# Kernel optimization log

Measured on AMD Instinct MI355X. Metric: run time of the kernel, lower is better.

## Reference

```python
import jax, jax.numpy as jnp
import numpy as np

N_NODES = 100000
N_EDGES = 1600000
D = 128
D_FF = 2 * D
BN_EPS = 1e-5


def setup_inputs() -> dict:
    key = jax.random.key(0)
    ks = jax.random.split(key, 16)
    s = lambda k, shp, fan: jax.random.normal(k, shp, jnp.float32) / np.float32(np.sqrt(fan))
    return {
        "x": jax.random.normal(ks[0], (N_NODES, D), jnp.float32),
        "edge_attr": jax.random.normal(ks[1], (N_EDGES, D), jnp.float32),
        "w1g": s(ks[2], (D, D), D),
        "b1g": jnp.zeros((D,), jnp.float32),
        "w2g": s(ks[3], (D, D), D),
        "b2g": jnp.zeros((D,), jnp.float32),
        "bn1_g": jax.random.uniform(ks[4], (D,), jnp.float32, 0.5, 1.5),
        "bn1_b": 0.1 * jax.random.normal(ks[5], (D,), jnp.float32),
        "ff_w1": s(ks[6], (D, D_FF), D),
        "ff_b1": jnp.zeros((D_FF,), jnp.float32),
        "ff_w2": s(ks[7], (D_FF, D), D_FF),
        "ff_b2": jnp.zeros((D,), jnp.float32),
        "bn2_g": jax.random.uniform(ks[8], (D,), jnp.float32, 0.5, 1.5),
        "bn2_b": 0.1 * jax.random.normal(ks[9], (D,), jnp.float32),
        "edge_index": jax.random.randint(ks[10], (2, N_EDGES), 0, N_NODES, jnp.int64 if jax.config.jax_enable_x64 else jnp.int32),
    }


def _batchnorm(h, gamma, beta):
    # training-mode BatchNorm1d: per-batch (node-axis) stats, biased variance
    mean = h.mean(axis=0)
    var = ((h - mean) ** 2).mean(axis=0)
    return gamma * (h - mean) * jax.lax.rsqrt(var + BN_EPS) + beta


def reference(x, edge_attr, w1g, b1g, w2g, b2g, bn1_g, bn1_b,
              ff_w1, ff_b1, ff_w2, ff_b2, bn2_g, bn2_b, edge_index):
    src, dst = edge_index[0], edge_index[1]
    # GINEConv message: relu(x_j + e_ij), scatter-sum into target nodes
    msg = jax.nn.relu(x[src] + edge_attr)                      # [E, D]
    agg = jax.ops.segment_sum(msg, dst, num_segments=N_NODES)  # [N, D]
    h = x + agg                                                # (1+eps)*x with eps=0
    # gin_nn: Linear -> ReLU -> Linear
    h = jax.nn.relu(h @ w1g + b1g) @ w2g + b2g
    h = jax.nn.relu(h)                                         # post-conv relu; dropout=identity (eval)
    h = x + h                                                  # residual
    h = _batchnorm(h, bn1_g, bn1_b)                            # norm1_local
    ff = jax.nn.relu(h @ ff_w1 + ff_b1) @ ff_w2 + ff_b2        # FFN block (dropouts identity)
    h = h + ff
    h = _batchnorm(h, bn2_g, bn2_b)                            # norm2
    return h
```

## Files before the change

### kernel.cpp

```cpp
#include <hip/hip_runtime.h>
#include <hip/hip_bf16.h>

#define NN 100000
#define NE 1600000
#define DD 128
#define DFF 256
#define BN_EPS 1e-5f
#define NND ((size_t)NN * DD)
#define NB_SCAN 391
#define NTILE 6250

typedef __attribute__((ext_vector_type(8))) short short8;
typedef __attribute__((ext_vector_type(4))) float f32x4;
typedef __attribute__((ext_vector_type(4))) unsigned short us4;

static __device__ __forceinline__ unsigned short f2bf(float f) {
  union { float f; unsigned u; } v; v.f = f;
  unsigned r = v.u + 0x7fffu + ((v.u >> 16) & 1u);
  return (unsigned short)(r >> 16);
}
static __device__ __forceinline__ float bf2f(unsigned short h) {
  union { unsigned u; float f; } v; v.u = ((unsigned)h) << 16;
  return v.f;
}

__global__ __launch_bounds__(256) void k_prep_misc(const float* __restrict__ x,
    unsigned short* __restrict__ xbf,
    const float* __restrict__ w1g, const float* __restrict__ w2g,
    const float* __restrict__ ffw1, const float* __restrict__ ffw2,
    unsigned short* __restrict__ w1t, unsigned short* __restrict__ w2t,
    unsigned short* __restrict__ fw1t, unsigned short* __restrict__ fw2t,
    const int* __restrict__ ei, int* __restrict__ cnt) {
  int b = blockIdx.x;
  if (b < 6250) {
    size_t base = ((size_t)b * 256u + threadIdx.x) * 8;
    const f32x4* xp = reinterpret_cast<const f32x4*>(x + base);
    f32x4 a0 = xp[0], a1 = xp[1];
    short8 o;
#pragma unroll
    for (int j = 0; j < 4; ++j) o[j] = (short)f2bf(a0[j]);
#pragma unroll
    for (int j = 0; j < 4; ++j) o[4 + j] = (short)f2bf(a1[j]);
    *reinterpret_cast<short8*>(xbf + base) = o;
  } else if (b < 6634) {
    int i = (b - 6250) * 256 + threadIdx.x;
    if (i < 16384) { int c = i & 127, k = i >> 7; w1t[c * 128 + k] = f2bf(w1g[k * 128 + c]); }
    else if (i < 32768) { i -= 16384; int c = i & 127, k = i >> 7; w2t[c * 128 + k] = f2bf(w2g[k * 128 + c]); }
    else if (i < 65536) { i -= 32768; int c = i & 255, k = i >> 8; fw1t[c * 128 + k] = f2bf(ffw1[k * 256 + c]); }
    else if (i < 98304) { i -= 65536; int c = i & 127, k = i >> 7; fw2t[c * 256 + k] = f2bf(ffw2[k * 128 + c]); }
  } else {
    int e = (b - 6634) * 256 + threadIdx.x;
    if (e < NE) atomicAdd(&cnt[ei[NE + e]], 1);
  }
}

__global__ __launch_bounds__(256) void k_scan1(const int* __restrict__ cnt,
                                               int* __restrict__ bsum) {
  __shared__ int sh[256];
  int n = blockIdx.x * 256 + threadIdx.x;
  sh[threadIdx.x] = (n < NN) ? cnt[n] : 0;
  __syncthreads();
  for (int off = 128; off > 0; off >>= 1) {
    if (threadIdx.x < off) sh[threadIdx.x] += sh[threadIdx.x + off];
    __syncthreads();
  }
  if (threadIdx.x == 0) bsum[blockIdx.x] = sh[0];
}

__global__ __launch_bounds__(512) void k_scan2(const int* __restrict__ bsum,
                                               int* __restrict__ bpre,
                                               int* __restrict__ rs,
                                               float* __restrict__ stats) {
  __shared__ int sh[512];
  int t = threadIdx.x;
  stats[t] = 0.f;
  int v = (t < NB_SCAN) ? bsum[t] : 0;
  sh[t] = v;
  __syncthreads();
  for (int off = 1; off < 512; off <<= 1) {
    int u = (t >= off) ? sh[t - off] : 0;
    __syncthreads();
    sh[t] += u;
    __syncthreads();
  }
  if (t < NB_SCAN) bpre[t] = sh[t] - v;
  if (t == NB_SCAN - 1) rs[NN] = sh[t];
}

__global__ __launch_bounds__(256) void k_scan3(int* __restrict__ rs,
                                               const int* __restrict__ bpre,
                                               int* __restrict__ cursor) {
  __shared__ int sh[256];
  int n = blockIdx.x * 256 + threadIdx.x;
  int t = threadIdx.x;
  int v = (n < NN) ? rs[n] : 0;
  sh[t] = v;
  __syncthreads();
  for (int off = 1; off < 256; off <<= 1) {
    int u = (t >= off) ? sh[t - off] : 0;
    __syncthreads();
    sh[t] += u;
    __syncthreads();
  }
  if (n < NN) {
    int ex = bpre[blockIdx.x] + sh[t] - v;
    rs[n] = ex;
    cursor[n] = ex;
  }
}

__global__ __launch_bounds__(256) void k_scatter(const int* __restrict__ ei,
                                                 int* __restrict__ cursor,
                                                 int2* __restrict__ el2) {
  int e = blockIdx.x * 256 + threadIdx.x;
  if (e >= NE) return;
  int s = ei[e], d = ei[NE + e];
  int p = atomicAdd(&cursor[d], 1);
  el2[p] = make_int2(e, s);
}

__global__ __launch_bounds__(256) void k_gather(
    const unsigned short* __restrict__ xbf, const float* __restrict__ ea,
    const int* __restrict__ rs, const int2* __restrict__ el2,
    unsigned short* __restrict__ h0) {
  int n = blockIdx.x * 8 + (threadIdx.x >> 5);
  int q = threadIdx.x & 31;
  int beg = rs[n], end = rs[n + 1];
  f32x4 acc = (f32x4){0.f, 0.f, 0.f, 0.f};
  int2 E0 = make_int2(0, 0), E1 = E0, E2 = E0, E3 = E0;
  int i = beg;
  if (i     < end) E0 = el2[i];
  if (i + 1 < end) E1 = el2[i + 1];
  if (i + 2 < end) E2 = el2[i + 2];
  if (i + 3 < end) E3 = el2[i + 3];
  for (; i + 4 <= end; i += 4) {
    f32x4 ev0 = *(reinterpret_cast<const f32x4*>(ea + (size_t)E0.x * DD) + q);
    us4  xv0 = *reinterpret_cast<const us4*>(xbf + (size_t)E0.y * DD + q * 4);
    f32x4 ev1 = *(reinterpret_cast<const f32x4*>(ea + (size_t)E1.x * DD) + q);
    us4  xv1 = *reinterpret_cast<const us4*>(xbf + (size_t)E1.y * DD + q * 4);
    f32x4 ev2 = *(reinterpret_cast<const f32x4*>(ea + (size_t)E2.x * DD) + q);
    us4  xv2 = *reinterpret_cast<const us4*>(xbf + (size_t)E2.y * DD + q * 4);
    f32x4 ev3 = *(reinterpret_cast<const f32x4*>(ea + (size_t)E3.x * DD) + q);
    us4  xv3 = *reinterpret_cast<const us4*>(xbf + (size_t)E3.y * DD + q * 4);
    int2 N0 = E0, N1 = E1, N2 = E2, N3 = E3;
    if (i + 4 < end) N0 = el2[i + 4];
    if (i + 5 < end) N1 = el2[i + 5];
    if (i + 6 < end) N2 = el2[i + 6];
    if (i + 7 < end) N3 = el2[i + 7];
#pragma unroll
    for (int c = 0; c < 4; ++c) {
      float m0 = bf2f((unsigned short)xv0[c]) + ev0[c];
      acc[c] += (m0 > 0.f) ? m0 : 0.f;
      float m1 = bf2f((unsigned short)xv1[c]) + ev1[c];
      acc[c] += (m1 > 0.f) ? m1 : 0.f;
      float m2 = bf2f((unsigned short)xv2[c]) + ev2[c];
      acc[c] += (m2 > 0.f) ? m2 : 0.f;
      float m3 = bf2f((unsigned short)xv3[c]) + ev3[c];
      acc[c] += (m3 > 0.f) ? m3 : 0.f;
    }
    E0 = N0; E1 = N1; E2 = N2; E3 = N3;
  }
  if (i < end) {
    f32x4 ev = *(reinterpret_cast<const f32x4*>(ea + (size_t)E0.x * DD) + q);
    us4  xv = *reinterpret_cast<const us4*>(xbf + (size_t)E0.y * DD + q * 4);
#pragma unroll
    for (int c = 0; c < 4; ++c) {
      float m = bf2f((unsigned short)xv[c]) + ev[c];
      acc[c] += (m > 0.f) ? m : 0.f;
    }
  }
  if (i + 1 < end) {
    f32x4 ev = *(reinterpret_cast<const f32x4*>(ea + (size_t)E1.x * DD) + q);
    us4  xv = *reinterpret_cast<const us4*>(xbf + (size_t)E1.y * DD + q * 4);
#pragma unroll
    for (int c = 0; c < 4; ++c) {
      float m = bf2f((unsigned short)xv[c]) + ev[c];
      acc[c] += (m > 0.f) ? m : 0.f;
    }
  }
  if (i + 2 < end) {
    f32x4 ev = *(reinterpret_cast<const f32x4*>(ea + (size_t)E2.x * DD) + q);
    us4  xv = *reinterpret_cast<const us4*>(xbf + (size_t)E2.y * DD + q * 4);
#pragma unroll
    for (int c = 0; c < 4; ++c) {
      float m = bf2f((unsigned short)xv[c]) + ev[c];
      acc[c] += (m > 0.f) ? m : 0.f;
    }
  }
  us4 xs = *reinterpret_cast<const us4*>(xbf + (size_t)n * DD + q * 4);
  union { unsigned short us[4]; unsigned long long u; } pk;
#pragma unroll
  for (int c = 0; c < 4; ++c) pk.us[c] = f2bf(bf2f((unsigned short)xs[c]) + acc[c]);
  *reinterpret_cast<unsigned long long*>(h0 + (size_t)n * DD + q * 4) = pk.u;
}

#define TR1 136
__global__ __launch_bounds__(256) void k_mlp1(const unsigned short* __restrict__ A,
    const unsigned short* __restrict__ W1T, const float* __restrict__ b1,
    const unsigned short* __restrict__ W2T, const float* __restrict__ b2,
    const unsigned short* __restrict__ xbf, float* __restrict__ O,
    float* __restrict__ stats) {
  __shared__ unsigned short w1s[16384];
  __shared__ unsigned short w2s[16384];
  __shared__ unsigned short tr[4][16 * TR1];
  __shared__ float lds_s[128], lds_q[128];
  int t = threadIdx.x;
  if (t < 128) { lds_s[t] = 0.f; lds_q[t] = 0.f; }
  {
    const short8* s1 = reinterpret_cast<const short8*>(W1T);
    const short8* s2 = reinterpret_cast<const short8*>(W2T);
    for (int i = t; i < 2048; i += 256) {
      int byte = i * 16;
      int c = byte >> 8;
      int sb = byte ^ ((c & 7) << 4);
      *reinterpret_cast<short8*>(reinterpret_cast<char*>(w1s) + sb) = s1[i];
      *reinterpret_cast<short8*>(reinterpret_cast<char*>(w2s) + sb) = s2[i];
    }
  }
  __syncthreads();
  int lane = t & 63, w = t >> 6;
  int l15 = lane & 15, g = lane >> 4;
  for (int tt = 0; tt < 4; ++tt) {
    int tile = blockIdx.x * 16 + w * 4 + tt;
    bool valid = tile < NTILE;
    int row0 = tile * 16;
    if (valid) {
      short8 a[4];
#pragma unroll
      for (int kt = 0; kt < 4; ++kt)
        a[kt] = *reinterpret_cast<const short8*>(A + (size_t)(row0 + l15) * DD + kt * 32 + g * 8);
      f32x4 acc[8];
#pragma unroll
      for (int ct = 0; ct < 8; ++ct) { float b = b1[ct * 16 + l15]; acc[ct] = (f32x4){b, b, b, b}; }
#pragma unroll
      for (int kt = 0; kt < 4; ++kt) {
        int k0 = kt * 32 + g * 8;
#pragma unroll
        for (int ct = 0; ct < 8; ++ct) {
          int c = ct * 16 + l15;
          int byte = ((c << 8) + k0 * 2) ^ ((c & 7) << 4);
          short8 b = *reinterpret_cast<const short8*>(reinterpret_cast<const char*>(w1s) + byte);
          acc[ct] = __builtin_amdgcn_mfma_f32_16x16x32_bf16(a[kt], b, acc[ct], 0, 0, 0);
        }
      }
#pragma unroll
      for (int ct = 0; ct < 8; ++ct)
#pragma unroll
        for (int r = 0; r < 4; ++r) {
          float v = acc[ct][r];
          v = v > 0.f ? v : 0.f;
          tr[w][(g * 4 + r) * TR1 + ct * 16 + l15] = f2bf(v);
        }
    }
    __syncthreads();
    if (valid) {
      short8 a2[4];
#pragma unroll
      for (int kt = 0; kt < 4; ++kt)
        a2[kt] = *reinterpret_cast<const short8*>(&tr[w][l15 * TR1 + kt * 32 + g * 8]);
      f32x4 acc2[8];
#pragma unroll
      for (int ct = 0; ct < 8; ++ct) { float b = b2[ct * 16 + l15]; acc2[ct] = (f32x4){b, b, b, b}; }
#pragma unroll
      for (int kt = 0; kt < 4; ++kt) {
        int k0 = kt * 32 + g * 8;
#pragma unroll
        for (int ct = 0; ct < 8; ++ct) {
          int c = ct * 16 + l15;
          int byte = ((c << 8) + k0 * 2) ^ ((c & 7) << 4);
          short8 b = *reinterpret_cast<const short8*>(reinterpret_cast<const char*>(w2s) + byte);
          acc2[ct] = __builtin_amdgcn_mfma_f32_16x16x32_bf16(a2[kt], b, acc2[ct], 0, 0, 0);
        }
      }
#pragma unroll
      for (int ct = 0; ct < 8; ++ct) {
        int c = ct * 16 + l15;
        float s = 0.f, q = 0.f;
#pragma unroll
        for (int r = 0; r < 4; ++r) {
          int row = row0 + g * 4 + r;
          float v = acc2[ct][r];
          v = v > 0.f ? v : 0.f;
          v += bf2f(xbf[(size_t)row * DD + c]);
          O[(size_t)row * DD + c] = v;
          s += v; q += v * v;
        }
        s += __shfl_xor(s, 16); s += __shfl_xor(s, 32);
        q += __shfl_xor(q, 16); q += __shfl_xor(q, 32);
        if (g == 0) { atomicAdd(&lds_s[c], s); atomicAdd(&lds_q[c], q); }
      }
    }
    __syncthreads();
  }
  if (t < 128) {
    atomicAdd(&stats[t], lds_s[t]);
    atomicAdd(&stats[128 + t], lds_q[t]);
  }
}

__global__ void k_bnfin(const float* __restrict__ st, const float* __restrict__ gm,
                        const float* __restrict__ bt, float* __restrict__ par) {
  int c = threadIdx.x;
  float mean = st[c] * (1.f / NN);
  float var = st[128 + c] * (1.f / NN) - mean * mean;
  float sc = gm[c] * rsqrtf(var + BN_EPS);
  par[c] = sc;
  par[128 + c] = bt[c] - mean * sc;
}

#define TR2 264
__global__ __launch_bounds__(256) void k_mlp2(const float* __restrict__ H,
    const float* __restrict__ par, const unsigned short* __restrict__ FW1T,
    const float* __restrict__ fb1, const unsigned short* __restrict__ FW2T,
    const float* __restrict__ fb2, float* __restrict__ O, float* __restrict__ stats) {
  __shared__ unsigned short fw1s[32768];
  __shared__ unsigned short tr[4][16 * TR2];
  __shared__ float lds_s[128], lds_q[128];
  int t = threadIdx.x;
  if (t < 128) { lds_s[t] = 0.f; lds_q[t] = 0.f; }
  {
    const short8* s1 = reinterpret_cast<const short8*>(FW1T);
    for (int i = t; i < 4096; i += 256) {
      int byte = i * 16;
      int c = byte >> 8;
      int sb = byte ^ ((c & 7) << 4);
      *reinterpret_cast<short8*>(reinterpret_cast<char*>(fw1s) + sb) = s1[i];
    }
  }
  __syncthreads();
  int lane = t & 63, w = t >> 6;
  int l15 = lane & 15, g = lane >> 4;
  for (int tt = 0; tt < 4; ++tt) {
    int tile = blockIdx.x * 16 + w * 4 + tt;
    bool valid = tile < NTILE;
    int row0 = tile * 16;
    if (valid) {
      const float* arow = H + (size_t)(row0 + l15) * DD;
      short8 a1[4];
#pragma unroll
      for (int kt = 0; kt < 4; ++kt) {
        int k0 = kt * 32 + g * 8;
        f32x4 u0 = *reinterpret_cast<const f32x4*>(arow + k0);
        f32x4 u1 = *reinterpret_cast<const f32x4*>(arow + k0 + 4);
        f32x4 sc0 = *reinterpret_cast<const f32x4*>(par + k0);
        f32x4 sc1 = *reinterpret_cast<const f32x4*>(par + k0 + 4);
        f32x4 sh0 = *reinterpret_cast<const f32x4*>(par + 128 + k0);
        f32x4 sh1 = *reinterpret_cast<const f32x4*>(par + 128 + k0 + 4);
        short8 af;
#pragma unroll
        for (int j = 0; j < 4; ++j) af[j] = (short)f2bf(sc0[j] * u0[j] + sh0[j]);
#pragma unroll
        for (int j = 0; j < 4; ++j) af[4 + j] = (short)f2bf(sc1[j] * u1[j] + sh1[j]);
        a1[kt] = af;
      }
      f32x4 acc1[16];
#pragma unroll
      for (int ct = 0; ct < 16; ++ct) { float b = fb1[ct * 16 + l15]; acc1[ct] = (f32x4){b, b, b, b}; }
#pragma unroll
      for (int kt = 0; kt < 4; ++kt) {
        int k0 = kt * 32 + g * 8;
#pragma unroll
        for (int ct = 0; ct < 16; ++ct) {
          int c = ct * 16 + l15;
          int byte = ((c << 8) + k0 * 2) ^ ((c & 7) << 4);
          short8 b = *reinterpret_cast<const short8*>(reinterpret_cast<const char*>(fw1s) + byte);
          acc1[ct] = __builtin_amdgcn_mfma_f32_16x16x32_bf16(a1[kt], b, acc1[ct], 0, 0, 0);
        }
      }
#pragma unroll
      for (int ct = 0; ct < 16; ++ct)
#pragma unroll
        for (int r = 0; r < 4; ++r) {
          float v = acc1[ct][r];
          v = v > 0.f ? v : 0.f;
          tr[w][(g * 4 + r) * TR2 + ct * 16 + l15] = f2bf(v);
        }
    }
    __syncthreads();
    if (valid) {
      short8 a2[8];
#pragma unroll
      for (int kt = 0; kt < 8; ++kt)
        a2[kt] = *reinterpret_cast<const short8*>(&tr[w][l15 * TR2 + kt * 32 + g * 8]);
      f32x4 acc2[8];
#pragma unroll
      for (int ct = 0; ct < 8; ++ct) { float b = fb2[ct * 16 + l15]; acc2[ct] = (f32x4){b, b, b, b}; }
#pragma unroll 2
      for (int kt = 0; kt < 8; ++kt) {
        int k0 = kt * 32 + g * 8;
#pragma unroll
        for (int ct = 0; ct < 8; ++ct) {
          int c = ct * 16 + l15;
          short8 b = *reinterpret_cast<const short8*>(FW2T + (size_t)c * DFF + k0);
          acc2[ct] = __builtin_amdgcn_mfma_f32_16x16x32_bf16(a2[kt], b, acc2[ct], 0, 0, 0);
        }
      }
#pragma unroll
      for (int ct = 0; ct < 8; ++ct) {
        int c = ct * 16 + l15;
        float sc = par[c], sh = par[128 + c];
        float s = 0.f, q = 0.f;
#pragma unroll
        for (int r = 0; r < 4; ++r) {
          int row = row0 + g * 4 + r;
          float h1v = sc * O[(size_t)row * DD + c] + sh;
          float v = acc2[ct][r] + h1v;
          O[(size_t)row * DD + c] = v;
          s += v; q += v * v;
        }
        s += __shfl_xor(s, 16); s += __shfl_xor(s, 32);
        q += __shfl_xor(q, 16); q += __shfl_xor(q, 32);
        if (g == 0) { atomicAdd(&lds_s[c], s); atomicAdd(&lds_q[c], q); }
      }
    }
    __syncthreads();
  }
  if (t < 128) {
    atomicAdd(&stats[t], lds_s[t]);
    atomicAdd(&stats[128 + t], lds_q[t]);
  }
}

__global__ __launch_bounds__(256) void k_bnfinal(float* __restrict__ h,
    const float* __restrict__ st, const float* __restrict__ gm,
    const float* __restrict__ bt) {
  size_t base = ((size_t)blockIdx.x * 256u + threadIdx.x) * 4;
  int c0 = (int)(base & 127);
  f32x4 v = *reinterpret_cast<f32x4*>(h + base);
#pragma unroll
  for (int j = 0; j < 4; ++j) {
    int c = c0 + j;
    float mean = st[c] * (1.f / NN);
    float var = st[128 + c] * (1.f / NN) - mean * mean;
    float sc = gm[c] * rsqrtf(var + BN_EPS);
    float sh = bt[c] - mean * sc;
    v[j] = sc * v[j] + sh;
  }
  *reinterpret_cast<f32x4*>(h + base) = v;
}

extern "C" void kernel_launch(void* const* d_in, const int* in_sizes, int n_in,
                              void* d_out, int out_size, void* d_ws, size_t ws_size,
                              hipStream_t stream) {
  const float* x    = (const float*)d_in[0];
  const float* ea   = (const float*)d_in[1];
  const float* w1g  = (const float*)d_in[2];
  const float* b1g  = (const float*)d_in[3];
  const float* w2g  = (const float*)d_in[4];
  const float* b2g  = (const float*)d_in[5];
  const float* bn1g = (const float*)d_in[6];
  const float* bn1b = (const float*)d_in[7];
  const float* ffw1 = (const float*)d_in[8];
  const float* ffb1 = (const float*)d_in[9];
  const float* ffw2 = (const float*)d_in[10];
  const float* ffb2 = (const float*)d_in[11];
  const float* bn2g = (const float*)d_in[12];
  const float* bn2b = (const float*)d_in[13];
  const int*   eidx = (const int*)d_in[14];
  float* out = (float*)d_out;

  char* ws = (char*)d_ws;
  int2* el2    = (int2*)(ws);
  int*  rs     = (int*)(ws + 12800000);
  int*  cursor = (int*)(ws + 13200128);
  int*  bsum   = (int*)(ws + 13600128);
  int*  bpre   = (int*)(ws + 13601728);
  float* stats = (float*)(ws + 13603328);
  float* par   = (float*)(ws + 13605376);
  unsigned short* w1t  = (unsigned short*)(ws + 13607424);
  unsigned short* w2t  = w1t + 16384;
  unsigned short* fw1t = w2t + 16384;
  unsigned short* fw2t = fw1t + 32768;
  unsigned short* xbf  = (unsigned short*)(ws + 13804032);
  unsigned short* hbf  = (unsigned short*)(ws + 39404032);

  hipMemsetAsync(rs, 0, (NN + 1) * 4, stream);

  k_prep_misc<<<12884, 256, 0, stream>>>(x, xbf, w1g, w2g, ffw1, ffw2,
                                         w1t, w2t, fw1t, fw2t, eidx, rs);

  k_scan1<<<NB_SCAN, 256, 0, stream>>>(rs, bsum);
  k_scan2<<<1, 512, 0, stream>>>(bsum, bpre, rs, stats);
  k_scan3<<<NB_SCAN, 256, 0, stream>>>(rs, bpre, cursor);
  k_scatter<<<6250, 256, 0, stream>>>(eidx, cursor, el2);

  k_gather<<<12500, 256, 0, stream>>>(xbf, ea, rs, el2, hbf);

  k_mlp1<<<391, 256, 0, stream>>>(hbf, w1t, b1g, w2t, b2g, xbf, out, stats);
  k_bnfin<<<1, 128, 0, stream>>>(stats, bn1g, bn1b, par);
  k_mlp2<<<391, 256, 0, stream>>>(out, par, fw1t, ffb1, fw2t, ffb2, out, stats + 256);
  k_bnfinal<<<12500, 256, 0, stream>>>(out, stats + 256, bn2g, bn2b);
}
```

Measured before the change: 745.7 us.

## Fuse preprocessing and MLP/BN stages into persistent kernels with grid barriers

Merges the memset, conversion, degree count, three-pass scan and scatter into one persistent kernel of 512 blocks separated by software grid barriers, and merges both MLPs, the BN-parameter finalisation and the final BN apply into a second persistent kernel. The aim is to remove many kernel launches and the gaps between them. In exchange it stops staging weights in LDS and reads them straight from global/L2 during the MFMA loops. It also relies on all 512 blocks being resident at once, since the spin barriers would otherwise deadlock.

```diff
diff --git a/kernel.cpp b/kernel.cpp
--- a/kernel.cpp
+++ b/kernel.cpp
@@ -7,8 +7,11 @@
 #define DFF 256
 #define BN_EPS 1e-5f
 #define NND ((size_t)NN * DD)
-#define NB_SCAN 391
 #define NTILE 6250
+#define GA 512
+#define GB 512
+#define TR1 136
+#define TR2 264
 
 typedef __attribute__((ext_vector_type(8))) short short8;
 typedef __attribute__((ext_vector_type(4))) float f32x4;
@@ -24,16 +27,38 @@
   return v.f;
 }
 
-__global__ __launch_bounds__(256) void k_prep_misc(const float* __restrict__ x,
-    unsigned short* __restrict__ xbf,
+static __device__ __forceinline__ void gsync(int* cnt, int nblk) {
+  __syncthreads();
+  if (threadIdx.x == 0) {
+    __threadfence();
+    __hip_atomic_fetch_add(cnt, 1, __ATOMIC_ACQ_REL, __HIP_MEMORY_SCOPE_AGENT);
+    while (__hip_atomic_load(cnt, __ATOMIC_ACQUIRE, __HIP_MEMORY_SCOPE_AGENT) < nblk)
+      __builtin_amdgcn_s_sleep(8);
+    __threadfence();
+  }
+  __syncthreads();
+}
+
+__global__ __launch_bounds__(256, 2) void k_megaA(
+    const float* __restrict__ x, unsigned short* __restrict__ xbf,
     const float* __restrict__ w1g, const float* __restrict__ w2g,
     const float* __restrict__ ffw1, const float* __restrict__ ffw2,
     unsigned short* __restrict__ w1t, unsigned short* __restrict__ w2t,
     unsigned short* __restrict__ fw1t, unsigned short* __restrict__ fw2t,
-    const int* __restrict__ ei, int* __restrict__ cnt) {
-  int b = blockIdx.x;
-  if (b < 6250) {
-    size_t base = ((size_t)b * 256u + threadIdx.x) * 8;
+    const int* __restrict__ ei, int* __restrict__ rs, int* __restrict__ cursor,
+    int* __restrict__ bsum, int* __restrict__ bpre, float* __restrict__ stats,
+    int2* __restrict__ el2, int* bar) {
+  __shared__ int sh[256];
+  int blk = blockIdx.x, t = threadIdx.x;
+  int gid = blk * 256 + t;
+  const int NT = GA * 256;
+
+  for (int i = gid; i <= NN; i += NT) rs[i] = 0;
+  if (gid < 512) stats[gid] = 0.f;
+  gsync(bar + 0, GA);
+
+  for (int i = gid; i < 1600000; i += NT) {
+    size_t base = (size_t)i * 8;
     const f32x4* xp = reinterpret_cast<const f32x4*>(x + base);
     f32x4 a0 = xp[0], a1 = xp[1];
     short8 o;
@@ -42,58 +67,18 @@
 #pragma unroll
     for (int j = 0; j < 4; ++j) o[4 + j] = (short)f2bf(a1[j]);
     *reinterpret_cast<short8*>(xbf + base) = o;
-  } else if (b < 6634) {
-    int i = (b - 6250) * 256 + threadIdx.x;
-    if (i < 16384) { int c = i & 127, k = i >> 7; w1t[c * 128 + k] = f2bf(w1g[k * 128 + c]); }
-    else if (i < 32768) { i -= 16384; int c = i & 127, k = i >> 7; w2t[c * 128 + k] = f2bf(w2g[k * 128 + c]); }
-    else if (i < 65536) { i -= 32768; int c = i & 255, k = i >> 8; fw1t[c * 128 + k] = f2bf(ffw1[k * 256 + c]); }
-    else if (i < 98304) { i -= 65536; int c = i & 127, k = i >> 7; fw2t[c * 256 + k] = f2bf(ffw2[k * 128 + c]); }
-  } else {
-    int e = (b - 6634) * 256 + threadIdx.x;
-    if (e < NE) atomicAdd(&cnt[ei[NE + e]], 1);
-  }
-}
-
-__global__ __launch_bounds__(256) void k_scan1(const int* __restrict__ cnt,
-                                               int* __restrict__ bsum) {
-  __shared__ int sh[256];
-  int n = blockIdx.x * 256 + threadIdx.x;
-  sh[threadIdx.x] = (n < NN) ? cnt[n] : 0;
-  __syncthreads();
-  for (int off = 128; off > 0; off >>= 1) {
-    if (threadIdx.x < off) sh[threadIdx.x] += sh[threadIdx.x + off];
-    __syncthreads();
-  }
-  if (threadIdx.x == 0) bsum[blockIdx.x] = sh[0];
-}
-
-__global__ __launch_bounds__(512) void k_scan2(const int* __restrict__ bsum,
-                                               int* __restrict__ bpre,
-                                               int* __restrict__ rs,
-                                               float* __restrict__ stats) {
-  __shared__ int sh[512];
-  int t = threadIdx.x;
-  stats[t] = 0.f;
-  int v = (t < NB_SCAN) ? bsum[t] : 0;
-  sh[t] = v;
-  __syncthreads();
-  for (int off = 1; off < 512; off <<= 1) {
-    int u = (t >= off) ? sh[t - off] : 0;
-    __syncthreads();
-    sh[t] += u;
-    __syncthreads();
-  }
-  if (t < NB_SCAN) bpre[t] = sh[t] - v;
-  if (t == NB_SCAN - 1) rs[NN] = sh[t];
-}
-
-__global__ __launch_bounds__(256) void k_scan3(int* __restrict__ rs,
-                                               const int* __restrict__ bpre,
-                                               int* __restrict__ cursor) {
-  __shared__ int sh[256];
-  int n = blockIdx.x * 256 + threadIdx.x;
-  int t = threadIdx.x;
-  int v = (n < NN) ? rs[n] : 0;
+  }
+  for (int i = gid; i < 98304; i += NT) {
+    int ii = i;
+    if (ii < 16384) { int c = ii & 127, k = ii >> 7; w1t[c * 128 + k] = f2bf(w1g[k * 128 + c]); }
+    else if (ii < 32768) { ii -= 16384; int c = ii & 127, k = ii >> 7; w2t[c * 128 + k] = f2bf(w2g[k * 128 + c]); }
+    else if (ii < 65536) { ii -= 32768; int c = ii & 255, k = ii >> 8; fw1t[c * 128 + k] = f2bf(ffw1[k * 256 + c]); }
+    else { ii -= 65536; int c = ii & 127, k = ii >> 7; fw2t[c * 256 + k] = f2bf(ffw2[k * 128 + c]); }
+  }
+  for (int e = gid; e < NE; e += NT) atomicAdd(&rs[ei[NE + e]], 1);
+  gsync(bar + 1, GA);
+
+  int v = (gid < NN) ? rs[gid] : 0;
   sh[t] = v;
   __syncthreads();
   for (int off = 1; off < 256; off <<= 1) {
@@ -102,21 +87,41 @@
     sh[t] += u;
     __syncthreads();
   }
-  if (n < NN) {
-    int ex = bpre[blockIdx.x] + sh[t] - v;
-    rs[n] = ex;
-    cursor[n] = ex;
-  }
-}
-
-__global__ __launch_bounds__(256) void k_scatter(const int* __restrict__ ei,
-                                                 int* __restrict__ cursor,
-                                                 int2* __restrict__ el2) {
-  int e = blockIdx.x * 256 + threadIdx.x;
-  if (e >= NE) return;
-  int s = ei[e], d = ei[NE + e];
-  int p = atomicAdd(&cursor[d], 1);
-  el2[p] = make_int2(e, s);
+  int incl = sh[t];
+  int ex = incl - v;
+  if (t == 255) bsum[blk] = incl;
+  gsync(bar + 2, GA);
+
+  if (blk == 0) {
+    int a0 = bsum[2 * t], a1 = bsum[2 * t + 1];
+    int ps = a0 + a1;
+    sh[t] = ps;
+    __syncthreads();
+    for (int off = 1; off < 256; off <<= 1) {
+      int u = (t >= off) ? sh[t - off] : 0;
+      __syncthreads();
+      sh[t] += u;
+      __syncthreads();
+    }
+    int excl = sh[t] - ps;
+    bpre[2 * t] = excl;
+    bpre[2 * t + 1] = excl + a0;
+    if (t == 255) rs[NN] = sh[255];
+  }
+  gsync(bar + 3, GA);
+
+  if (gid < NN) {
+    int e0 = bpre[blk] + ex;
+    rs[gid] = e0;
+    cursor[gid] = e0;
+  }
+  gsync(bar + 4, GA);
+
+  for (int e = gid; e < NE; e += NT) {
+    int s = ei[e], d = ei[NE + e];
+    int p = atomicAdd(&cursor[d], 1);
+    el2[p] = make_int2(e, s);
+  }
 }
 
 __global__ __launch_bounds__(256) void k_gather(
@@ -194,249 +199,206 @@
   *reinterpret_cast<unsigned long long*>(h0 + (size_t)n * DD + q * 4) = pk.u;
 }
 
-#define TR1 136
-__global__ __launch_bounds__(256) void k_mlp1(const unsigned short* __restrict__ A,
+__global__ __launch_bounds__(256, 2) void k_megaB(
+    const unsigned short* __restrict__ hbf,
     const unsigned short* __restrict__ W1T, const float* __restrict__ b1,
     const unsigned short* __restrict__ W2T, const float* __restrict__ b2,
     const unsigned short* __restrict__ xbf, float* __restrict__ O,
-    float* __restrict__ stats) {
-  __shared__ unsigned short w1s[16384];
-  __shared__ unsigned short w2s[16384];
-  __shared__ unsigned short tr[4][16 * TR1];
-  __shared__ float lds_s[128], lds_q[128];
+    float* __restrict__ stats,
+    const float* __restrict__ bn1g, const float* __restrict__ bn1b,
+    const unsigned short* __restrict__ FW1T, const float* __restrict__ fb1,
+    const unsigned short* __restrict__ FW2T, const float* __restrict__ fb2,
+    const float* __restrict__ bn2g, const float* __restrict__ bn2b, int* bar) {
+  __shared__ unsigned short trb[4][16 * TR2];
+  __shared__ float lds_s[128], lds_q[128], ldspar[256];
   int t = threadIdx.x;
-  if (t < 128) { lds_s[t] = 0.f; lds_q[t] = 0.f; }
-  {
-    const short8* s1 = reinterpret_cast<const short8*>(W1T);
-    const short8* s2 = reinterpret_cast<const short8*>(W2T);
-    for (int i = t; i < 2048; i += 256) {
-      int byte = i * 16;
-      int c = byte >> 8;
-      int sb = byte ^ ((c & 7) << 4);
-      *reinterpret_cast<short8*>(reinterpret_cast<char*>(w1s) + sb) = s1[i];
-      *reinterpret_cast<short8*>(reinterpret_cast<char*>(w2s) + sb) = s2[i];
-    }
-  }
-  __syncthreads();
   int lane = t & 63, w = t >> 6;
   int l15 = lane & 15, g = lane >> 4;
-  for (int tt = 0; tt < 4; ++tt) {
-    int tile = blockIdx.x * 16 + w * 4 + tt;
-    bool valid = tile < NTILE;
+  int wid = blockIdx.x * 4 + w;
+  if (t < 128) { lds_s[t] = 0.f; lds_q[t] = 0.f; }
+  __syncthreads();
+
+  for (int tile = wid; tile < NTILE; tile += GB * 4) {
     int row0 = tile * 16;
-    if (valid) {
-      short8 a[4];
-#pragma unroll
-      for (int kt = 0; kt < 4; ++kt)
-        a[kt] = *reinterpret_cast<const short8*>(A + (size_t)(row0 + l15) * DD + kt * 32 + g * 8);
-      f32x4 acc[8];
-#pragma unroll
-      for (int ct = 0; ct < 8; ++ct) { float b = b1[ct * 16 + l15]; acc[ct] = (f32x4){b, b, b, b}; }
-#pragma unroll
-      for (int kt = 0; kt < 4; ++kt) {
-        int k0 = kt * 32 + g * 8;
-#pragma unroll
-        for (int ct = 0; ct < 8; ++ct) {
-          int c = ct * 16 + l15;
-          int byte = ((c << 8) + k0 * 2) ^ ((c & 7) << 4);
-          short8 b = *reinterpret_cast<const short8*>(reinterpret_cast<const char*>(w1s) + byte);
-          acc[ct] = __builtin_amdgcn_mfma_f32_16x16x32_bf16(a[kt], b, acc[ct], 0, 0, 0);
-        }
-      }
-#pragma unroll
-      for (int ct = 0; ct < 8; ++ct)
-#pragma unroll
-        for (int r = 0; r < 4; ++r) {
-          float v = acc[ct][r];
-          v = v > 0.f ? v : 0.f;
-          tr[w][(g * 4 + r) * TR1 + ct * 16 + l15] = f2bf(v);
-        }
-    }
-    __syncthreads();
-    if (valid) {
-      short8 a2[4];
-#pragma unroll
-      for (int kt = 0; kt < 4; ++kt)
-        a2[kt] = *reinterpret_cast<const short8*>(&tr[w][l15 * TR1 + kt * 32 + g * 8]);
-      f32x4 acc2[8];
-#pragma unroll
-      for (int ct = 0; ct < 8; ++ct) { float b = b2[ct * 16 + l15]; acc2[ct] = (f32x4){b, b, b, b}; }
-#pragma unroll
-      for (int kt = 0; kt < 4; ++kt) {
-        int k0 = kt * 32 + g * 8;
-#pragma unroll
-        for (int ct = 0; ct < 8; ++ct) {
-          int c = ct * 16 + l15;
-          int byte = ((c << 8) + k0 * 2) ^ ((c & 7) << 4);
-          short8 b = *reinterpret_cast<const short8*>(reinterpret_cast<const char*>(w2s) + byte);
-          acc2[ct] = __builtin_amdgcn_mfma_f32_16x16x32_bf16(a2[kt], b, acc2[ct], 0, 0, 0);
-        }
-      }
+    f32x4 acc[8];
+#pragma unroll
+    for (int ct = 0; ct < 8; ++ct) { float b = b1[ct * 16 + l15]; acc[ct] = (f32x4){b, b, b, b}; }
+    short8 a[4];
+#pragma unroll
+    for (int kt = 0; kt < 4; ++kt)
+      a[kt] = *reinterpret_cast<const short8*>(hbf + (size_t)(row0 + l15) * DD + kt * 32 + g * 8);
+#pragma unroll
+    for (int kt = 0; kt < 4; ++kt) {
+      int k0 = kt * 32 + g * 8;
 #pragma unroll
       for (int ct = 0; ct < 8; ++ct) {
         int c = ct * 16 + l15;
-        float s = 0.f, q = 0.f;
-#pragma unroll
-        for (int r = 0; r < 4; ++r) {
-          int row = row0 + g * 4 + r;
-          float v = acc2[ct][r];
-          v = v > 0.f ? v : 0.f;
-          v += bf2f(xbf[(size_t)row * DD + c]);
-          O[(size_t)row * DD + c] = v;
-          s += v; q += v * v;
-        }
-        s += __shfl_xor(s, 16); s += __shfl_xor(s, 32);
-        q += __shfl_xor(q, 16); q += __shfl_xor(q, 32);
-        if (g == 0) { atomicAdd(&lds_s[c], s); atomicAdd(&lds_q[c], q); }
-      }
-    }
-    __syncthreads();
-  }
+        short8 b = *reinterpret_cast<const short8*>(W1T + (size_t)c * DD + k0);
+        acc[ct] = __builtin_amdgcn_mfma_f32_16x16x32_bf16(a[kt], b, acc[ct], 0, 0, 0);
+      }
+    }
+#pragma unroll
+    for (int ct = 0; ct < 8; ++ct)
+#pragma unroll
+      for (int r = 0; r < 4; ++r) {
+        float v = acc[ct][r];
+        v = v > 0.f ? v : 0.f;
+        trb[w][(g * 4 + r) * TR1 + ct * 16 + l15] = f2bf(v);
+      }
+    short8 a2[4];
+#pragma unroll
+    for (int kt = 0; kt < 4; ++kt)
+      a2[kt] = *reinterpret_cast<const short8*>(&trb[w][l15 * TR1 + kt * 32 + g * 8]);
+    f32x4 acc2[8];
+#pragma unroll
+    for (int ct = 0; ct < 8; ++ct) { float b = b2[ct * 16 + l15]; acc2[ct] = (f32x4){b, b, b, b}; }
+#pragma unroll
+    for (int kt = 0; kt < 4; ++kt) {
+      int k0 = kt * 32 + g * 8;
+#pragma unroll
+      for (int ct = 0; ct < 8; ++ct) {
+        int c = ct * 16 + l15;
+        short8 b = *reinterpret_cast<const short8*>(W2T + (size_t)c * DD + k0);
+        acc2[ct] = __builtin_amdgcn_mfma_f32_16x16x32_bf16(a2[kt], b, acc2[ct], 0, 0, 0);
+      }
+    }
+#pragma unroll
+    for (int ct = 0; ct < 8; ++ct) {
+      int c = ct * 16 + l15;
+      float s = 0.f, q = 0.f;
+#pragma unroll
+      for (int r = 0; r < 4; ++r) {
+        int row = row0 + g * 4 + r;
+        float v = acc2[ct][r];
+        v = v > 0.f ? v : 0.f;
+        v += bf2f(xbf[(size_t)row * DD + c]);
+        O[(size_t)row * DD + c] = v;
+        s += v; q += v * v;
+      }
+      s += __shfl_xor(s, 16); s += __shfl_xor(s, 32);
+      q += __shfl_xor(q, 16); q += __shfl_xor(q, 32);
+      if (g == 0) { atomicAdd(&lds_s[c], s); atomicAdd(&lds_q[c], q); }
+    }
+  }
+  __syncthreads();
   if (t < 128) {
     atomicAdd(&stats[t], lds_s[t]);
     atomicAdd(&stats[128 + t], lds_q[t]);
-  }
-}
-
-__global__ void k_bnfin(const float* __restrict__ st, const float* __restrict__ gm,
-                        const float* __restrict__ bt, float* __restrict__ par) {
-  int c = threadIdx.x;
-  float mean = st[c] * (1.f / NN);
-  float var = st[128 + c] * (1.f / NN) - mean * mean;
-  float sc = gm[c] * rsqrtf(var + BN_EPS);
-  par[c] = sc;
-  par[128 + c] = bt[c] - mean * sc;
-}
-
-#define TR2 264
-__global__ __launch_bounds__(256) void k_mlp2(const float* __restrict__ H,
-    const float* __restrict__ par, const unsigned short* __restrict__ FW1T,
-    const float* __restrict__ fb1, const unsigned short* __restrict__ FW2T,
-    const float* __restrict__ fb2, float* __restrict__ O, float* __restrict__ stats) {
-  __shared__ unsigned short fw1s[32768];
-  __shared__ unsigned short tr[4][16 * TR2];
-  __shared__ float lds_s[128], lds_q[128];
-  int t = threadIdx.x;
-  if (t < 128) { lds_s[t] = 0.f; lds_q[t] = 0.f; }
-  {
-    const short8* s1 = reinterpret_cast<const short8*>(FW1T);
-    for (int i = t; i < 4096; i += 256) {
-      int byte = i * 16;
-      int c = byte >> 8;
-      int sb = byte ^ ((c & 7) << 4);
-      *reinterpret_cast<short8*>(reinterpret_cast<char*>(fw1s) + sb) = s1[i];
-    }
-  }
-  __syncthreads();
-  int lane = t & 63, w = t >> 6;
-  int l15 = lane & 15, g = lane >> 4;
-  for (int tt = 0; tt < 4; ++tt) {
-    int tile = blockIdx.x * 16 + w * 4 + tt;
-    bool valid = tile < NTILE;
+    lds_s[t] = 0.f; lds_q[t] = 0.f;
+  }
+  gsync(bar + 5, GB);
+
+  if (t < 128) {
+    float mean = stats[t] * (1.f / NN);
+    float var = stats[128 + t] * (1.f / NN) - mean * mean;
+    float sc = bn1g[t] * rsqrtf(var + BN_EPS);
+    ldspar[t] = sc;
+    ldspar[128 + t] = bn1b[t] - mean * sc;
+  }
+  __syncthreads();
+
+  for (int tile = wid; tile < NTILE; tile += GB * 4) {
     int row0 = tile * 16;
-    if (valid) {
-      const float* arow = H + (size_t)(row0 + l15) * DD;
-      short8 a1[4];
-#pragma unroll
-      for (int kt = 0; kt < 4; ++kt) {
-        int k0 = kt * 32 + g * 8;
-        f32x4 u0 = *reinterpret_cast<const f32x4*>(arow + k0);
-        f32x4 u1 = *reinterpret_cast<const f32x4*>(arow + k0 + 4);
-        f32x4 sc0 = *reinterpret_cast<const f32x4*>(par + k0);
-        f32x4 sc1 = *reinterpret_cast<const f32x4*>(par + k0 + 4);
-        f32x4 sh0 = *reinterpret_cast<const f32x4*>(par + 128 + k0);
-        f32x4 sh1 = *reinterpret_cast<const f32x4*>(par + 128 + k0 + 4);
-        short8 af;
-#pragma unroll
-        for (int j = 0; j < 4; ++j) af[j] = (short)f2bf(sc0[j] * u0[j] + sh0[j]);
-#pragma unroll
-        for (int j = 0; j < 4; ++j) af[4 + j] = (short)f2bf(sc1[j] * u1[j] + sh1[j]);
-        a1[kt] = af;
-      }
-      f32x4 acc1[16];
-#pragma unroll
-      for (int ct = 0; ct < 16; ++ct) { float b = fb1[ct * 16 + l15]; acc1[ct] = (f32x4){b, b, b, b}; }
-#pragma unroll
-      for (int kt = 0; kt < 4; ++kt) {
-        int k0 = kt * 32 + g * 8;
-#pragma unroll
-        for (int ct = 0; ct < 16; ++ct) {
-          int c = ct * 16 + l15;
-          int byte = ((c << 8) + k0 * 2) ^ ((c & 7) << 4);
-          short8 b = *reinterpret_cast<const short8*>(reinterpret_cast<const char*>(fw1s) + byte);
-          acc1[ct] = __builtin_amdgcn_mfma_f32_16x16x32_bf16(a1[kt], b, acc1[ct], 0, 0, 0);
-        }
-      }
-#pragma unroll
-      for (int ct = 0; ct < 16; ++ct)
-#pragma unroll
-        for (int r = 0; r < 4; ++r) {
-          float v = acc1[ct][r];
-          v = v > 0.f ? v : 0.f;
-          tr[w][(g * 4 + r) * TR2 + ct * 16 + l15] = f2bf(v);
-        }
-    }
-    __syncthreads();
-    if (valid) {
-      short8 a2[8];
-#pragma unroll
-      for (int kt = 0; kt < 8; ++kt)
-        a2[kt] = *reinterpret_cast<const short8*>(&tr[w][l15 * TR2 + kt * 32 + g * 8]);
-      f32x4 acc2[8];
-#pragma unroll
-      for (int ct = 0; ct < 8; ++ct) { float b = fb2[ct * 16 + l15]; acc2[ct] = (f32x4){b, b, b, b}; }
+    const float* arow = O + (size_t)(row0 + l15) * DD;
+    short8 a1[4];
+#pragma unroll
+    for (int kt = 0; kt < 4; ++kt) {
+      int k0 = kt * 32 + g * 8;
+      f32x4 u0 = *reinterpret_cast<const f32x4*>(arow + k0);
+      f32x4 u1 = *reinterpret_cast<const f32x4*>(arow + k0 + 4);
+      short8 af;
+#pragma unroll
+      for (int j = 0; j < 4; ++j)
+        af[j] = (short)f2bf(ldspar[k0 + j] * u0[j] + ldspar[128 + k0 + j]);
+#pragma unroll
+      for (int j = 0; j < 4; ++j)
+        af[4 + j] = (short)f2bf(ldspar[k0 + 4 + j] * u1[j] + ldspar[128 + k0 + 4 + j]);
+      a1[kt] = af;
+    }
+    f32x4 acc1[16];
+#pragma unroll
+    for (int ct = 0; ct < 16; ++ct) { float b = fb1[ct * 16 + l15]; acc1[ct] = (f32x4){b, b, b, b}; }
+#pragma unroll
+    for (int kt = 0; kt < 4; ++kt) {
+      int k0 = kt * 32 + g * 8;
+#pragma unroll
+      for (int ct = 0; ct < 16; ++ct) {
+        int c = ct * 16 + l15;
+        short8 b = *reinterpret_cast<const short8*>(FW1T + (size_t)c * DD + k0);
+        acc1[ct] = __builtin_amdgcn_mfma_f32_16x16x32_bf16(a1[kt], b, acc1[ct], 0, 0, 0);
+      }
+    }
+#pragma unroll
+    for (int ct = 0; ct < 16; ++ct)
+#pragma unroll
+      for (int r = 0; r < 4; ++r) {
+        float v = acc1[ct][r];
+        v = v > 0.f ? v : 0.f;
+        trb[w][(g * 4 + r) * TR2 + ct * 16 + l15] = f2bf(v);
+      }
+    short8 a2[8];
+#pragma unroll
+    for (int kt = 0; kt < 8; ++kt)
+      a2[kt] = *reinterpret_cast<const short8*>(&trb[w][l15 * TR2 + kt * 32 + g * 8]);
+    f32x4 acc2[8];
+#pragma unroll
+    for (int ct = 0; ct < 8; ++ct) { float b = fb2[ct * 16 + l15]; acc2[ct] = (f32x4){b, b, b, b}; }
 #pragma unroll 2
-      for (int kt = 0; kt < 8; ++kt) {
-        int k0 = kt * 32 + g * 8;
-#pragma unroll
-        for (int ct = 0; ct < 8; ++ct) {
-          int c = ct * 16 + l15;
-          short8 b = *reinterpret_cast<const short8*>(FW2T + (size_t)c * DFF + k0);
-          acc2[ct] = __builtin_amdgcn_mfma_f32_16x16x32_bf16(a2[kt], b, acc2[ct], 0, 0, 0);
-        }
-      }
+    for (int kt = 0; kt < 8; ++kt) {
+      int k0 = kt * 32 + g * 8;
 #pragma unroll
       for (int ct = 0; ct < 8; ++ct) {
         int c = ct * 16 + l15;
-        float sc = par[c], sh = par[128 + c];
-        float s = 0.f, q = 0.f;
-#pragma unroll
-        for (int r = 0; r < 4; ++r) {
-          int row = row0 + g * 4 + r;
-          float h1v = sc * O[(size_t)row * DD + c] + sh;
-          float v = acc2[ct][r] + h1v;
-          O[(size_t)row * DD + c] = v;
-          s += v; q += v * v;
-        }
-        s += __shfl_xor(s, 16); s += __shfl_xor(s, 32);
-        q += __shfl_xor(q, 16); q += __shfl_xor(q, 32);
-        if (g == 0) { atomicAdd(&lds_s[c], s); atomicAdd(&lds_q[c], q); }
-      }
-    }
-    __syncthreads();
-  }
+        short8 b = *reinterpret_cast<const short8*>(FW2T + (size_t)c * DFF + k0);
+        acc2[ct] = __builtin_amdgcn_mfma_f32_16x16x32_bf16(a2[kt], b, acc2[ct], 0, 0, 0);
+      }
+    }
+#pragma unroll
+    for (int ct = 0; ct < 8; ++ct) {
+      int c = ct * 16 + l15;
+      float sc = ldspar[c], shv = ldspar[128 + c];
+      float s = 0.f, q = 0.f;
+#pragma unroll
+      for (int r = 0; r < 4; ++r) {
+        int row = row0 + g * 4 + r;
+        float h1v = sc * O[(size_t)row * DD + c] + shv;
+        float v = acc2[ct][r] + h1v;
+        O[(size_t)row * DD + c] = v;
+        s += v; q += v * v;
+      }
+      s += __shfl_xor(s, 16); s += __shfl_xor(s, 32);
+      q += __shfl_xor(q, 16); q += __shfl_xor(q, 32);
+      if (g == 0) { atomicAdd(&lds_s[c], s); atomicAdd(&lds_q[c], q); }
+    }
+  }
+  __syncthreads();
   if (t < 128) {
-    atomicAdd(&stats[t], lds_s[t]);
-    atomicAdd(&stats[128 + t], lds_q[t]);
-  }
-}
-
-__global__ __launch_bounds__(256) void k_bnfinal(float* __restrict__ h,
-    const float* __restrict__ st, const float* __restrict__ gm,
-    const float* __restrict__ bt) {
-  size_t base = ((size_t)blockIdx.x * 256u + threadIdx.x) * 4;
-  int c0 = (int)(base & 127);
-  f32x4 v = *reinterpret_cast<f32x4*>(h + base);
-#pragma unroll
-  for (int j = 0; j < 4; ++j) {
-    int c = c0 + j;
-    float mean = st[c] * (1.f / NN);
-    float var = st[128 + c] * (1.f / NN) - mean * mean;
-    float sc = gm[c] * rsqrtf(var + BN_EPS);
-    float sh = bt[c] - mean * sc;
-    v[j] = sc * v[j] + sh;
-  }
-  *reinterpret_cast<f32x4*>(h + base) = v;
+    atomicAdd(&stats[256 + t], lds_s[t]);
+    atomicAdd(&stats[384 + t], lds_q[t]);
+  }
+  gsync(bar + 6, GB);
+
+  {
+    int gid = blockIdx.x * 256 + t;
+    int cb = (gid & 31) * 4;
+    f32x4 sc4, sh4;
+#pragma unroll
+    for (int j = 0; j < 4; ++j) {
+      int c = cb + j;
+      float mean = stats[256 + c] * (1.f / NN);
+      float var = stats[384 + c] * (1.f / NN) - mean * mean;
+      float sc = bn2g[c] * rsqrtf(var + BN_EPS);
+      sc4[j] = sc;
+      sh4[j] = bn2b[c] - mean * sc;
+    }
+    for (int idx = gid; idx < 3200000; idx += GB * 256) {
+      f32x4* p = reinterpret_cast<f32x4*>(O + (size_t)idx * 4);
+      f32x4 v = *p;
+#pragma unroll
+      for (int j = 0; j < 4; ++j) v[j] = sc4[j] * v[j] + sh4[j];
+      *p = v;
+    }
+  }
 }
 
 extern "C" void kernel_launch(void* const* d_in, const int* in_sizes, int n_in,
@@ -464,30 +426,25 @@
   int*  rs     = (int*)(ws + 12800000);
   int*  cursor = (int*)(ws + 13200128);
   int*  bsum   = (int*)(ws + 13600128);
-  int*  bpre   = (int*)(ws + 13601728);
-  float* stats = (float*)(ws + 13603328);
-  float* par   = (float*)(ws + 13605376);
-  unsigned short* w1t  = (unsigned short*)(ws + 13607424);
-  unsigned short* w2t  = w1t + 16384;
-  unsigned short* fw1t = w2t + 16384;
-  unsigned short* fw2t = fw1t + 32768;
-  unsigned short* xbf  = (unsigned short*)(ws + 13804032);
-  unsigned short* hbf  = (unsigned short*)(ws + 39404032);
-
-  hipMemsetAsync(rs, 0, (NN + 1) * 4, stream);
-
-  k_prep_misc<<<12884, 256, 0, stream>>>(x, xbf, w1g, w2g, ffw1, ffw2,
-                                         w1t, w2t, fw1t, fw2t, eidx, rs);
-
-  k_scan1<<<NB_SCAN, 256, 0, stream>>>(rs, bsum);
-  k_scan2<<<1, 512, 0, stream>>>(bsum, bpre, rs, stats);
-  k_scan3<<<NB_SCAN, 256, 0, stream>>>(rs, bpre, cursor);
-  k_scatter<<<6250, 256, 0, stream>>>(eidx, cursor, el2);
+  int*  bpre   = (int*)(ws + 13602176);
+  float* stats = (float*)(ws + 13604224);
+  int*  bar    = (int*)(ws + 13606272);
+  unsigned short* w1t  = (unsigned short*)(ws + 13606400);
+  unsigned short* w2t  = (unsigned short*)(ws + 13639168);
+  unsigned short* fw1t = (unsigned short*)(ws + 13671936);
+  unsigned short* fw2t = (unsigned short*)(ws + 13737472);
+  unsigned short* xbf  = (unsigned short*)(ws + 13803008);
+  unsigned short* hbf  = (unsigned short*)(ws + 39403008);
+
+  hipMemsetAsync(bar, 0, 64, stream);
+
+  k_megaA<<<GA, 256, 0, stream>>>(x, xbf, w1g, w2g, ffw1, ffw2,
+                                  w1t, w2t, fw1t, fw2t, eidx, rs, cursor,
+                                  bsum, bpre, stats, el2, bar);
 
   k_gather<<<12500, 256, 0, stream>>>(xbf, ea, rs, el2, hbf);
 
-  k_mlp1<<<391, 256, 0, stream>>>(hbf, w1t, b1g, w2t, b2g, xbf, out, stats);
-  k_bnfin<<<1, 128, 0, stream>>>(stats, bn1g, bn1b, par);
-  k_mlp2<<<391, 256, 0, stream>>>(out, par, fw1t, ffb1, fw2t, ffb2, out, stats + 256);
-  k_bnfinal<<<12500, 256, 0, stream>>>(out, stats + 256, bn2g, bn2b);
-}
+  k_megaB<<<GB, 256, 0, stream>>>(hbf, w1t, b1g, w2t, b2g, xbf, out, stats,
+                                  bn1g, bn1b, fw1t, ffb1, fw2t, ffb2,
+                                  bn2g, bn2b, bar);
+}
```

Result: slower. 1.405 ms (+88.4%).
